# Optimization experiments

Hardware: AMD Instinct MI355X
Metric: run time of the kernel (lower is better)

Reference implementation:

```python
import jax, jax.numpy as jnp
import numpy as np

B, L, H, N = 32, 4096, 256, 512
THR = 0.0          # sim_threshold
NEG = -1e9         # mask value for softmax
SLOPE = 0.2        # LeakyReLU negative slope
EPS = 1e-8         # torch cosine_similarity eps


def _span_mean(cs, st, ed):
    # cs: [B, L+1, H] inclusive prefix sums with leading zero row
    hi = jnp.take_along_axis(cs, (ed + 1)[:, :, None], axis=1)  # [B,N,H]
    lo = jnp.take_along_axis(cs, st[:, :, None], axis=1)
    cnt = (ed - st + 1).astype(cs.dtype)[:, :, None]
    return (hi - lo) / cnt


def _leaky(x):
    return jnp.where(x >= 0, x, SLOPE * x)


def _forward(embeddings, W_trip, b_trip, edge_emb, W_attn, b_attn, W_gat, b_gat,
             asp_st, asp_len, opi_st, opi_len, sent_id):
    Bv, Lv, Hv = embeddings.shape
    asp_ed = asp_st + asp_len  # [B,N], always < L by construction
    opi_ed = opi_st + opi_len

    # span means via prefix sums (replaces per-triplet slice .mean(0))
    cs = jnp.concatenate([jnp.zeros((Bv, 1, Hv), embeddings.dtype),
                          jnp.cumsum(embeddings, axis=1)], axis=1)  # [B,L+1,H]
    asp_repr = _span_mean(cs, asp_st, asp_ed)  # [B,N,H]
    opi_repr = _span_mean(cs, opi_st, opi_ed)
    sent_vec = jax.nn.one_hot(sent_id, 3, dtype=embeddings.dtype)  # [B,N,3]

    node_in = jnp.concatenate([asp_repr, opi_repr, sent_vec], axis=-1)  # [B,N,2H+3]
    node = node_in @ W_trip + b_trip  # [B,N,H] triplet_proj

    # pairwise cosine similarity (torch eps semantics)
    nrm = jnp.sqrt(jnp.sum(node * node, axis=-1))  # [B,N]
    dots = jnp.einsum('bih,bjh->bij', node, node)
    sim = dots / jnp.maximum(nrm[:, :, None] * nrm[:, None, :], EPS)  # [B,N,N]

    eye = jnp.eye(N, dtype=bool)[None]
    same_asp = (asp_st[:, :, None] == asp_st[:, None, :]) & (asp_ed[:, :, None] == asp_ed[:, None, :])
    same_opi = (opi_st[:, :, None] == opi_st[:, None, :]) & (opi_ed[:, :, None] == opi_ed[:, None, :])
    pass_sim = (sim > THR) & ~eye
    mask0 = pass_sim & same_asp  # edge (src=i, tgt=j), type 0
    mask1 = pass_sim & same_opi  # type 1
    # em[b, tgt, src, type]
    em = jnp.stack([jnp.swapaxes(mask0, 1, 2), jnp.swapaxes(mask1, 1, 2)], axis=-1)

    # attn_fc(leaky_relu(concat[node_tgt, node_src, edge_emb])) decomposes linearly
    lnode = _leaky(node)            # [B,N,H]
    ledge = _leaky(edge_emb)        # [2,H]
    a_tgt = (lnode @ W_attn[:H]).squeeze(-1)        # [B,N]
    a_src = (lnode @ W_attn[H:2 * H]).squeeze(-1)   # [B,N]
    a_e = (ledge @ W_attn[2 * H:]).squeeze(-1)      # [2]
    score = (a_tgt[:, :, None, None] + a_src[:, None, :, None]
             + a_e[None, None, None, :] + b_attn[0])  # [B,N,N,2]

    masked = jnp.where(em, score, NEG)
    w = jax.nn.softmax(masked.reshape(Bv, N, -1), axis=-1).reshape(Bv, N, N, 2)
    w = w * em.astype(w.dtype)  # exact zeros on non-edges / neighborless rows

    # aggregate msgs = concat[node_src, edge_emb[type]]
    w_node = w.sum(-1)                                   # [B,tgt,src]
    agg_node = jnp.einsum('bki,bih->bkh', w_node, node)  # [B,N,H]
    agg_e = w.sum(2) @ edge_emb                          # [B,N,H]
    agg = jnp.concatenate([agg_node, agg_e], axis=-1)    # [B,N,2H]
    upd = jax.nn.relu(agg @ W_gat + b_gat)               # gat_proj + relu

    has_neigh = em.any(axis=(2, 3))                      # [B,N]
    node_out = jnp.where(has_neigh[:, :, None], upd, node)

    # original skips the whole batch element if it has no edges at all
    b_has_edge = em.any(axis=(1, 2, 3))                  # [B]
    node_add = jnp.where(b_has_edge[:, None, None], node_out, 0.0)

    center = (asp_st + opi_st) // 2                      # [B,N], < L
    b_idx = jnp.broadcast_to(jnp.arange(Bv)[:, None], center.shape)
    enhanced = embeddings.at[b_idx, center].add(node_add)
    return enhanced


def setup_inputs() -> dict:
    key = jax.random.key(0)
    ks = jax.random.split(key, 12)
    embeddings = jax.random.normal(ks[0], (B, L, H), jnp.float32)
    W_trip = jax.random.normal(ks[1], (2 * H + 3, H), jnp.float32) * 0.05
    b_trip = jnp.zeros((H,), jnp.float32)
    edge_emb = jax.random.normal(ks[2], (2, H), jnp.float32) * 0.05
    W_attn = jax.random.normal(ks[3], (3 * H, 1), jnp.float32) * 0.05
    b_attn = jnp.zeros((1,), jnp.float32)
    W_gat = jax.random.normal(ks[4], (2 * H, H), jnp.float32) * 0.05
    b_gat = jnp.zeros((H,), jnp.float32)
    asp_st = jax.random.randint(ks[5], (B, N), 0, 128, dtype=jnp.int32)
    asp_len = jax.random.randint(ks[6], (B, N), 0, 8, dtype=jnp.int32)
    opi_st = jax.random.randint(ks[7], (B, N), 0, 128, dtype=jnp.int32)
    opi_len = jax.random.randint(ks[8], (B, N), 0, 8, dtype=jnp.int32)
    sent_id = jax.random.randint(ks[9], (B, N), 0, 3, dtype=jnp.int32)
    return dict(embeddings=embeddings, W_trip=W_trip, b_trip=b_trip, edge_emb=edge_emb,
                W_attn=W_attn, b_attn=b_attn, W_gat=W_gat, b_gat=b_gat,
                asp_st=asp_st, asp_len=asp_len, opi_st=opi_st, opi_len=opi_len,
                sent_id=sent_id)


def reference(embeddings, W_trip, b_trip, edge_emb, W_attn, b_attn, W_gat, b_gat,
              asp_st, asp_len, opi_st, opi_len, sent_id):
    return _forward(embeddings, W_trip, b_trip, edge_emb, W_attn, b_attn, W_gat, b_gat,
                    asp_st, asp_len, opi_st, opi_len, sent_id)
```

## Files before the change

### kernel.cpp

```cpp
#include <hip/hip_runtime.h>
#include <hip/hip_bf16.h>
#include <math.h>

#define Bn 32
#define Ln 4096
#define ROWS 16384
#define LR 136
#define SLOPEC 0.2f
#define NEGSENT -1e30f

typedef __attribute__((ext_vector_type(8))) short bf16x8;
typedef __attribute__((ext_vector_type(4))) float f32x4;

__device__ __forceinline__ void copy_lin(const float* __restrict__ emb,
        float* __restrict__ out, long start, int count, int tid) {
    const f32x4* s4 = (const f32x4*)emb;
    f32x4* d4 = (f32x4*)out;
    for (int i = tid; i < count; i += 256)
        d4[start + i] = s4[start + i];
}

__device__ __forceinline__ f32x4 leaky4(f32x4 v) {
    f32x4 r;
    r.x = v.x >= 0.f ? v.x : SLOPEC * v.x;
    r.y = v.y >= 0.f ? v.y : SLOPEC * v.y;
    r.z = v.z >= 0.f ? v.z : SLOPEC * v.z;
    r.w = v.w >= 0.f ? v.w : SLOPEC * v.w;
    return r;
}

__global__ __launch_bounds__(256) void k_pre(const float* __restrict__ Wtrip,
        const float* __restrict__ btrip, const float* __restrict__ Eemb,
        const float* __restrict__ Wattn, const float* __restrict__ Wgat,
        const int* __restrict__ ast, const int* __restrict__ alen,
        const int* __restrict__ ost, const int* __restrict__ olen,
        const float* __restrict__ emb, float* __restrict__ out,
        __hip_bfloat16* __restrict__ WtGT, __hip_bfloat16* __restrict__ embh,
        float* __restrict__ W3g, float* __restrict__ btg,
        float* __restrict__ ae, float* __restrict__ ve,
        int* __restrict__ keys, int* __restrict__ bflag) {
    int bid = blockIdx.x, tid = threadIdx.x;
    copy_lin(emb, out, (long)bid * 864, 864, tid);
    __shared__ float Als[32][68];
    __shared__ float Bls[32][64];
    __shared__ float red[4];
    __shared__ float vr0[8][32], vr1[8][32];
    if (bid < 32) {
        int mat = bid >> 4, t = bid & 15;
        int m0 = (t >> 2) << 6, n0 = (t & 3) << 6;
        const float* A = Wtrip + mat * 65536;
        int r0 = (tid & 15) << 2, c0 = (tid >> 4) << 2;
        float acc[4][4] = {};
        for (int kk = 0; kk < 256; kk += 32) {
            __syncthreads();
            #pragma unroll
            for (int p = 0; p < 2; ++p) {
                int idx = tid + (p << 8);
                int row = idx >> 3, kq = (idx & 7) << 2;
                const float4 v = *(const float4*)(A + (size_t)(m0 + row) * 256 + kk + kq);
                Als[kq + 0][row] = v.x; Als[kq + 1][row] = v.y;
                Als[kq + 2][row] = v.z; Als[kq + 3][row] = v.w;
            }
            #pragma unroll
            for (int p = 0; p < 2; ++p) {
                int idx = tid + (p << 8);
                int k = idx >> 4, hq = (idx & 15) << 2;
                *(float4*)(&Bls[k][hq]) = *(const float4*)(Wgat + (size_t)(kk + k) * 256 + n0 + hq);
            }
            __syncthreads();
            #pragma unroll
            for (int k = 0; k < 32; ++k) {
                float4 a  = *(const float4*)(&Als[k][r0]);
                float4 bv = *(const float4*)(&Bls[k][c0]);
                acc[0][0] += a.x*bv.x; acc[0][1] += a.x*bv.y; acc[0][2] += a.x*bv.z; acc[0][3] += a.x*bv.w;
                acc[1][0] += a.y*bv.x; acc[1][1] += a.y*bv.y; acc[1][2] += a.y*bv.z; acc[1][3] += a.y*bv.w;
                acc[2][0] += a.z*bv.x; acc[2][1] += a.z*bv.y; acc[2][2] += a.z*bv.z; acc[2][3] += a.z*bv.w;
                acc[3][0] += a.w*bv.x; acc[3][1] += a.w*bv.y; acc[3][2] += a.w*bv.z; acc[3][3] += a.w*bv.w;
            }
        }
        #pragma unroll
        for (int i = 0; i < 4; ++i)
            #pragma unroll
            for (int j = 0; j < 4; ++j)
                WtGT[(size_t)(mat * 256 + n0 + c0 + j) * 256 + m0 + r0 + i] =
                    __float2bfloat16(acc[i][j]);
    } else if (bid == 32) {
        float s = 0.f;
        for (int k = 0; k < 256; ++k) s += btrip[k] * Wgat[(size_t)k * 256 + tid];
        btg[tid] = s;
    } else if (bid == 33) {
        if (tid < Bn) bflag[tid] = 0;
        #pragma unroll
        for (int e = 0; e < 2; ++e) {
            float x = Eemb[e * 256 + tid];
            float lx = x >= 0.f ? x : SLOPEC * x;
            float s = lx * Wattn[512 + tid];
            #pragma unroll
            for (int o = 32; o; o >>= 1) s += __shfl_down(s, o);
            if ((tid & 63) == 0) red[tid >> 6] = s;
            __syncthreads();
            if (tid == 0) ae[e] = red[0] + red[1] + red[2] + red[3];
            __syncthreads();
        }
    } else if (bid < 37) {
        int s = bid - 34;
        float acc = 0.f;
        for (int k = 0; k < 256; ++k)
            acc += Wtrip[(size_t)(512 + s) * 256 + k] * Wgat[(size_t)k * 256 + tid];
        W3g[s * 256 + tid] = acc;
    } else if (bid < 45) {
        int j = bid - 37;
        int n0 = j << 5;
        int nl = tid & 31, kg = tid >> 5;
        float p0 = 0.f, p1 = 0.f;
        for (int kk = 0; kk < 32; ++kk) {
            int k = (kg << 5) + kk;
            float w = Wgat[(size_t)(256 + k) * 256 + n0 + nl];
            p0 += Eemb[k] * w;
            p1 += Eemb[256 + k] * w;
        }
        vr0[kg][nl] = p0; vr1[kg][nl] = p1;
        __syncthreads();
        if (tid < 32) {
            float s0 = 0.f, s1 = 0.f;
            #pragma unroll
            for (int g = 0; g < 8; ++g) { s0 += vr0[g][tid]; s1 += vr1[g][tid]; }
            ve[n0 + tid] = s0;
            ve[256 + n0 + tid] = s1;
        }
    } else if (bid < 109) {
        int row = (bid - 45) * 256 + tid;
        keys[row] = (((ast[row] << 3) | alen[row]) << 10) | ((ost[row] << 3) | olen[row]);
    } else if (bid < 126) {
        int rbase = (bid - 109) << 8;
        int b2 = rbase / LR, l2 = rbase - b2 * LR;
        for (int r = 0; r < 256; ++r) {
            embh[(size_t)(rbase + r) * 256 + tid] =
                __float2bfloat16(emb[((size_t)b2 * Ln + l2) * 256 + tid]);
            if (++l2 == LR) { l2 = 0; ++b2; }
        }
    }
}

__global__ __launch_bounds__(256) void k_pq(const float* __restrict__ emb,
        const float* __restrict__ Wtrip,
        const __hip_bfloat16* __restrict__ embh, const __hip_bfloat16* __restrict__ WtGT,
        float* __restrict__ PQ, float* __restrict__ PQ2, float* __restrict__ out) {
    __shared__ float Als[32][68];
    __shared__ float Bls[32][64];
    int tid = threadIdx.x;
    int bid = blockIdx.x;
    copy_lin(emb, out, 884736L + (long)bid * 2048, 2048, tid);

    if (bid < 544) {
        int m0 = (bid % 68) << 6;
        int j = bid / 68;
        const float* Bp = Wtrip + ((j < 4) ? (j << 6) : (65536 + ((j - 4) << 6)));
        int r0 = (tid & 15) << 2;
        int c0 = (tid >> 4) << 2;
        float acc[4][4] = {};
        for (int kk = 0; kk < 256; kk += 32) {
            __syncthreads();
            #pragma unroll
            for (int p = 0; p < 2; ++p) {
                int idx = tid + (p << 8);
                int row = idx >> 3;
                int kq = (idx & 7) << 2;
                int m = m0 + row;
                int b = m / LR;
                int l = m - b * LR;
                const float4 v = *(const float4*)(emb + (size_t)(b * Ln + l) * 256 + kk + kq);
                Als[kq + 0][row] = v.x; Als[kq + 1][row] = v.y;
                Als[kq + 2][row] = v.z; Als[kq + 3][row] = v.w;
            }
            #pragma unroll
            for (int p = 0; p < 2; ++p) {
                int idx = tid + (p << 8);
                int k = idx >> 4;
                int hq = (idx & 15) << 2;
                *(float4*)(&Bls[k][hq]) = *(const float4*)(Bp + (size_t)(kk + k) * 256 + hq);
            }
            __syncthreads();
            #pragma unroll
            for (int k = 0; k < 32; ++k) {
                float4 a  = *(const float4*)(&Als[k][r0]);
                float4 bv = *(const float4*)(&Bls[k][c0]);
                acc[0][0] += a.x*bv.x; acc[0][1] += a.x*bv.y; acc[0][2] += a.x*bv.z; acc[0][3] += a.x*bv.w;
                acc[1][0] += a.y*bv.x; acc[1][1] += a.y*bv.y; acc[1][2] += a.y*bv.z; acc[1][3] += a.y*bv.w;
                acc[2][0] += a.z*bv.x; acc[2][1] += a.z*bv.y; acc[2][2] += a.z*bv.z; acc[2][3] += a.z*bv.w;
                acc[3][0] += a.w*bv.x; acc[3][1] += a.w*bv.y; acc[3][2] += a.w*bv.z; acc[3][3] += a.w*bv.w;
            }
        }
        #pragma unroll
        for (int i = 0; i < 4; ++i)
            #pragma unroll
            for (int jj = 0; jj < 4; ++jj)
                PQ[(size_t)(m0 + r0 + i) * 512 + (j << 6) + c0 + jj] = acc[i][jj];
    } else {
        int bb = bid - 544;
        int wave = tid >> 6, lane = tid & 63;
        int m0 = ((bb % 68) << 6) + (wave << 4);
        int n0 = (bb / 68) << 6;
        int fr = lane & 15;
        int kq = (lane >> 4) << 3;
        f32x4 acc[4] = {};
        for (int k0 = 0; k0 < 256; k0 += 32) {
            bf16x8 a = *(const bf16x8*)(embh + (size_t)(m0 + fr) * 256 + k0 + kq);
            #pragma unroll
            for (int nf = 0; nf < 4; ++nf) {
                bf16x8 b = *(const bf16x8*)(WtGT + (size_t)(n0 + (nf << 4) + fr) * 256 + k0 + kq);
                acc[nf] = __builtin_amdgcn_mfma_f32_16x16x32_bf16(a, b, acc[nf], 0, 0, 0);
            }
        }
        int r0 = (lane >> 4) << 2;
        #pragma unroll
        for (int nf = 0; nf < 4; ++nf)
            #pragma unroll
            for (int r = 0; r < 4; ++r)
                PQ2[(size_t)(m0 + r0 + r) * 512 + n0 + (nf << 4) + fr] = acc[nf][r];
    }
}

__global__ __launch_bounds__(256) void k_combine(const float* __restrict__ PQ,
        const float* __restrict__ PQ2,
        const float* __restrict__ Wtrip, const float* __restrict__ btrip,
        const int* __restrict__ sid,
        const int* __restrict__ ast, const int* __restrict__ alen,
        const int* __restrict__ ost, const int* __restrict__ olen,
        const float* __restrict__ Wattn, const float* __restrict__ W3g,
        const float* __restrict__ btg, const float* __restrict__ emb,
        float* __restrict__ out, float* __restrict__ node, float* __restrict__ nodeW,
        float* __restrict__ atg, float* __restrict__ asr) {
    int bid = blockIdx.x, tid = threadIdx.x;
    int wv = tid >> 6, lane = tid & 63;
    copy_lin(emb, out, 3112960L + (long)bid * 512, 512, tid);

    int row = (bid << 2) + wv;
    int b = row >> 9;
    int as_ = ast[row], al = alen[row];
    int os_ = ost[row], ol = olen[row];
    int c = lane << 2;
    const float* Pb  = PQ  + (size_t)b * LR * 512 + c;
    const float* Pb2 = PQ2 + (size_t)b * LR * 512 + c;

    f32x4 asum = {0.f,0.f,0.f,0.f}, osum = asum, p2 = asum, q2 = asum;
    for (int i = 0; i <= al; ++i) {
        size_t off = (size_t)(as_ + i) * 512;
        asum += *(const f32x4*)(Pb + off);
        p2   += *(const f32x4*)(Pb2 + off);
    }
    for (int i = 0; i <= ol; ++i) {
        size_t off = (size_t)(os_ + i) * 512 + 256;
        osum += *(const f32x4*)(Pb + off);
        q2   += *(const f32x4*)(Pb2 + off);
    }
    float ra = 1.f / (float)(al + 1), ro = 1.f / (float)(ol + 1);
    int sd = sid[row];

    f32x4 x = asum * ra + osum * ro
            + *(const f32x4*)(Wtrip + (size_t)(512 + sd) * 256 + c)
            + *(const f32x4*)(btrip + c);
    *(f32x4*)(node + (size_t)row * 256 + c) = x;

    f32x4 nw = p2 * ra + q2 * ro
             + *(const f32x4*)(W3g + sd * 256 + c)
             + *(const f32x4*)(btg + c);
    *(f32x4*)(nodeW + (size_t)row * 256 + c) = nw;

    f32x4 lx = leaky4(x);
    f32x4 w1 = *(const f32x4*)(Wattn + c);
    f32x4 w2 = *(const f32x4*)(Wattn + 256 + c);
    float s1 = lx.x*w1.x + lx.y*w1.y + lx.z*w1.z + lx.w*w1.w;
    float s2 = lx.x*w2.x + lx.y*w2.y + lx.z*w2.z + lx.w*w2.w;
    #pragma unroll
    for (int o = 32; o; o >>= 1) {
        s1 += __shfl_xor(s1, o);
        s2 += __shfl_xor(s2, o);
    }
    if (lane == 0) { atg[row] = s1; asr[row] = s2; }
}

__global__ __launch_bounds__(256) void k_edges(
        const float* __restrict__ node, const float* __restrict__ nodeW,
        const float* __restrict__ atg, const float* __restrict__ asr,
        const float* __restrict__ ae, const float* __restrict__ battn,
        const float* __restrict__ ve, const float* __restrict__ bgat,
        const int* __restrict__ keys,
        const float* __restrict__ emb, float* __restrict__ out,
        float* __restrict__ nadd, int* __restrict__ bflag) {
    int bid = blockIdx.x;
    int tid = threadIdx.x;
    int wv = tid >> 6, lane = tid & 63;

    copy_lin(emb, out, 5210112L + (long)bid * 776, 776, tid);

    int tgt = (bid << 2) + wv;
    int b = tgt >> 9, base = b << 9, lt = tgt & 511;

    int mykey = keys[tgt];
    int ka = mykey >> 10, ko = mykey & 1023;

    unsigned long long mA[8], mO[8];
    #pragma unroll
    for (int j = 0; j < 8; ++j) {
        int ls = (j << 6) + lane;
        int k2 = keys[base + ls];
        bool self = (ls == lt);
        mA[j] = __ballot(((k2 >> 10) == ka) && !self);
        mO[j] = __ballot(((k2 & 1023) == ko) && !self);
    }

    f32x4 xt4 = *(const f32x4*)(node + (size_t)tgt * 256 + (lane << 2));
    float a_t = atg[tgt];
    float ae0 = ae[0], ae1 = ae[1], b0 = battn[0];

    float s0a[8], s1a[8];
    unsigned long long mK[8];
    #pragma unroll
    for (int j = 0; j < 8; ++j) {
        s0a[j] = NEGSENT; s1a[j] = NEGSENT;
        unsigned long long m = mA[j] | mO[j];
        while (m) {
            int bit = __builtin_ctzll(m); m &= m - 1;
            int gs = base + (j << 6) + bit;
            f32x4 y = *(const f32x4*)(node + (size_t)gs * 256 + (lane << 2));
            float p = xt4.x * y.x + xt4.y * y.y + xt4.z * y.z + xt4.w * y.w;
            #pragma unroll
            for (int o = 32; o; o >>= 1) p += __shfl_xor(p, o);
            if (p > 0.f && lane == bit) {
                float bs = a_t + asr[gs] + b0;
                if ((mA[j] >> bit) & 1) s0a[j] = bs + ae0;
                if ((mO[j] >> bit) & 1) s1a[j] = bs + ae1;
            }
        }
        mK[j] = __ballot(s0a[j] > -1e29f || s1a[j] > -1e29f);
    }

    float mx = NEGSENT;
    #pragma unroll
    for (int j = 0; j < 8; ++j) mx = fmaxf(mx, fmaxf(s0a[j], s1a[j]));
    #pragma unroll
    for (int o = 32; o; o >>= 1) mx = fmaxf(mx, __shfl_xor(mx, o));
    bool has = mx > -1e29f;

    float se0 = 0.f, se1 = 0.f;
    #pragma unroll
    for (int j = 0; j < 8; ++j) {
        se0 += expf(s0a[j] - mx);
        se1 += expf(s1a[j] - mx);
    }
    #pragma unroll
    for (int o = 32; o; o >>= 1) { se0 += __shfl_xor(se0, o); se1 += __shfl_xor(se1, o); }
    float rden = 1.f / (se0 + se1);

    f32x4 res;
    if (has) {
        f32x4 agg4 = {0.f, 0.f, 0.f, 0.f};
        #pragma unroll
        for (int j = 0; j < 8; ++j) {
            unsigned long long m = mK[j];
            while (m) {
                int bit = __builtin_ctzll(m); m &= m - 1;
                int gs = base + (j << 6) + bit;
                float w0 = __shfl(s0a[j], bit);
                float w1 = __shfl(s1a[j], bit);
                float wt = (expf(w0 - mx) + expf(w1 - mx)) * rden;
                const f32x4 nw = *(const f32x4*)(nodeW + (size_t)gs * 256 + (lane << 2));
                agg4.x += wt * nw.x; agg4.y += wt * nw.y;
                agg4.z += wt * nw.z; agg4.w += wt * nw.w;
            }
        }
        f32x4 v1 = *(const f32x4*)(ve + (lane << 2));
        f32x4 v2 = *(const f32x4*)(ve + 256 + (lane << 2));
        f32x4 bg = *(const f32x4*)(bgat + (lane << 2));
        float c0 = se0 * rden, c1 = se1 * rden;
        res.x = fmaxf(agg4.x + c0 * v1.x + c1 * v2.x + bg.x, 0.f);
        res.y = fmaxf(agg4.y + c0 * v1.y + c1 * v2.y + bg.y, 0.f);
        res.z = fmaxf(agg4.z + c0 * v1.z + c1 * v2.z + bg.z, 0.f);
        res.w = fmaxf(agg4.w + c0 * v1.w + c1 * v2.w + bg.w, 0.f);
        if (lane == 0) bflag[b] = 1;
    } else {
        res = xt4;
    }
    *(f32x4*)(nadd + (size_t)tgt * 256 + (lane << 2)) = res;
}

__global__ __launch_bounds__(256) void k_scatter(const float* __restrict__ emb,
        const float* __restrict__ nadd,
        const int* __restrict__ ast, const int* __restrict__ ost,
        const int* __restrict__ bflag, float* __restrict__ out) {
    int b = blockIdx.x >> 7;
    int r = blockIdx.x & 127;
    int tid = threadIdx.x;

    __shared__ int cen[512];
    __shared__ unsigned long long s_mask[8];
    for (int n = tid; n < 512; n += 256)
        cen[n] = (ast[(b << 9) + n] + ost[(b << 9) + n]) >> 1;
    __syncthreads();
    #pragma unroll
    for (int p = 0; p < 2; ++p) {
        int n = tid + (p << 8);
        unsigned long long bal = __ballot(cen[n] == r);
        if ((tid & 63) == 0) s_mask[(p << 2) + (tid >> 6)] = bal;
    }
    __syncthreads();
    size_t o = ((size_t)b * Ln + r) * 256 + tid;
    float acc = emb[o];
    if (bflag[b]) {
        for (int w = 0; w < 8; ++w) {
            unsigned long long m = s_mask[w];
            while (m) {
                int n = (w << 6) + __builtin_ctzll(m); m &= m - 1;
                acc += nadd[((size_t)(b << 9) + n) * 256 + tid];
            }
        }
    }
    out[o] = acc;
}

extern "C" void kernel_launch(void* const* d_in, const int* in_sizes, int n_in,
                              void* d_out, int out_size, void* d_ws, size_t ws_size,
                              hipStream_t stream) {
    const float* emb   = (const float*)d_in[0];
    const float* Wtrip = (const float*)d_in[1];
    const float* btrip = (const float*)d_in[2];
    const float* Eemb  = (const float*)d_in[3];
    const float* Wattn = (const float*)d_in[4];
    const float* battn = (const float*)d_in[5];
    const float* Wgat  = (const float*)d_in[6];
    const float* bgat  = (const float*)d_in[7];
    const int* ast  = (const int*)d_in[8];
    const int* alen = (const int*)d_in[9];
    const int* ost  = (const int*)d_in[10];
    const int* olen = (const int*)d_in[11];
    const int* sid  = (const int*)d_in[12];
    float* out = (float*)d_out;

    float* ws    = (float*)d_ws;
    float* PQ    = ws;
    float* PQ2   = PQ + (size_t)4352 * 512;
    float* node  = PQ2 + (size_t)4352 * 512;
    float* nodeW = node + (size_t)ROWS * 256;
    float* nadd  = nodeW + (size_t)ROWS * 256;
    float* W3g   = nadd + (size_t)ROWS * 256;
    float* btg   = W3g + 768;
    float* atg   = btg + 256;
    float* asr   = atg + ROWS;
    float* ae    = asr + ROWS;
    float* ve    = ae + 2;
    int* bflag   = (int*)(ve + 512);
    int* keys    = bflag + Bn;
    __hip_bfloat16* embh = (__hip_bfloat16*)(keys + ROWS + 32);
    __hip_bfloat16* WtGT = embh + (size_t)4352 * 256;

    k_pre<<<1024, 256, 0, stream>>>(Wtrip, btrip, Eemb, Wattn, Wgat,
                                    ast, alen, ost, olen, emb, out,
                                    WtGT, embh, W3g, btg, ae, ve, keys, bflag);
    k_pq<<<1088, 256, 0, stream>>>(emb, Wtrip, embh, WtGT, PQ, PQ2, out);
    k_combine<<<ROWS / 4, 256, 0, stream>>>(PQ, PQ2, Wtrip, btrip, sid,
                                            ast, alen, ost, olen,
                                            Wattn, W3g, btg, emb, out, node, nodeW,
                                            atg, asr);
    k_edges<<<ROWS / 4, 256, 0, stream>>>(node, nodeW, atg, asr, ae, battn, ve, bgat,
                                          keys, emb, out, nadd, bflag);
    k_scatter<<<Bn * 128, 256, 0, stream>>>(emb, nadd, ast, ost, bflag, out);
}
```

Baseline: 157.9 us.

## Fuse scatter into edge kernel via atomics and repartition output copy

Removes the separate scatter kernel and the nadd buffer: each target row's updated node vector is atomically added into the output at its span-center row. The copy of embeddings into the output is redistributed so the first 128 rows per batch are copied before k_edges runs. A small fix-up kernel subtracts node contributions for batches with no edges. k_combine and k_edges blocks are also remapped to interleave batches. This trades a full extra kernel pass and nadd traffic for float atomics, which are contended on shared center rows and make the summation order nondeterministic.

New measurement: 179.0 us. 1.13x slower.

```diff
diff --git a/kernel.cpp b/kernel.cpp
--- a/kernel.cpp
+++ b/kernel.cpp
@@ -40,7 +40,20 @@
         float* __restrict__ ae, float* __restrict__ ve,
         int* __restrict__ keys, int* __restrict__ bflag) {
     int bid = blockIdx.x, tid = threadIdx.x;
-    copy_lin(emb, out, (long)bid * 864, 864, tid);
+    copy_lin(emb, out, (long)bid * 1536, 1536, tid);
+    {
+        const f32x4* s4 = (const f32x4*)emb;
+        f32x4* d4 = (f32x4*)out;
+        #pragma unroll
+        for (int i = 0; i < 64; i += 256) {}
+        int s2base = bid * 64;
+        #pragma unroll
+        for (int i = tid; i < 64; i += 256) {
+            long s2 = s2base + i;
+            long slot = ((24L + (s2 >> 13)) << 18) | (s2 & 8191);
+            d4[slot] = s4[slot];
+        }
+    }
     __shared__ float Als[32][68];
     __shared__ float Bls[32][64];
     __shared__ float red[4];
@@ -150,7 +163,7 @@
     __shared__ float Bls[32][64];
     int tid = threadIdx.x;
     int bid = blockIdx.x;
-    copy_lin(emb, out, 884736L + (long)bid * 2048, 2048, tid);
+    copy_lin(emb, out, 1572864L + (long)bid * 2048, 2048, tid);
 
     if (bid < 544) {
         int m0 = (bid % 68) << 6;
@@ -233,9 +246,10 @@
         float* __restrict__ atg, float* __restrict__ asr) {
     int bid = blockIdx.x, tid = threadIdx.x;
     int wv = tid >> 6, lane = tid & 63;
-    copy_lin(emb, out, 3112960L + (long)bid * 512, 512, tid);
-
-    int row = (bid << 2) + wv;
+    copy_lin(emb, out, 3801088L + (long)bid * 608, 608, tid);
+
+    int s = ((bid & 7) << 9) | (bid >> 3);
+    int row = (s << 2) + wv;
     int b = row >> 9;
     int as_ = ast[row], al = alen[row];
     int os_ = ost[row], ol = olen[row];
@@ -286,15 +300,23 @@
         const float* __restrict__ ae, const float* __restrict__ battn,
         const float* __restrict__ ve, const float* __restrict__ bgat,
         const int* __restrict__ keys,
+        const int* __restrict__ ast, const int* __restrict__ ost,
         const float* __restrict__ emb, float* __restrict__ out,
-        float* __restrict__ nadd, int* __restrict__ bflag) {
+        int* __restrict__ bflag) {
     int bid = blockIdx.x;
     int tid = threadIdx.x;
     int wv = tid >> 6, lane = tid & 63;
 
-    copy_lin(emb, out, 5210112L + (long)bid * 776, 776, tid);
-
-    int tgt = (bid << 2) + wv;
+    {
+        const f32x4* s4 = (const f32x4*)emb;
+        f32x4* d4 = (f32x4*)out;
+        long base = ((24L + (bid >> 9)) << 18) + 8192 + (long)(bid & 511) * 496;
+        for (int i = tid; i < 496; i += 256)
+            d4[base + i] = s4[base + i];
+    }
+
+    int s = ((bid & 7) << 9) | (bid >> 3);
+    int tgt = (s << 2) + wv;
     int b = tgt >> 9, base = b << 9, lt = tgt & 511;
 
     int mykey = keys[tgt];
@@ -382,41 +404,26 @@
     } else {
         res = xt4;
     }
-    *(f32x4*)(nadd + (size_t)tgt * 256 + (lane << 2)) = res;
-}
-
-__global__ __launch_bounds__(256) void k_scatter(const float* __restrict__ emb,
-        const float* __restrict__ nadd,
+    int cen = (ast[tgt] + ost[tgt]) >> 1;
+    float* orow = out + ((size_t)b * Ln + cen) * 256 + (lane << 2);
+    atomicAdd(orow + 0, res.x);
+    atomicAdd(orow + 1, res.y);
+    atomicAdd(orow + 2, res.z);
+    atomicAdd(orow + 3, res.w);
+}
+
+__global__ __launch_bounds__(256) void k_fix(const float* __restrict__ node,
         const int* __restrict__ ast, const int* __restrict__ ost,
         const int* __restrict__ bflag, float* __restrict__ out) {
-    int b = blockIdx.x >> 7;
-    int r = blockIdx.x & 127;
+    int b = blockIdx.x;
+    if (bflag[b]) return;
     int tid = threadIdx.x;
-
-    __shared__ int cen[512];
-    __shared__ unsigned long long s_mask[8];
-    for (int n = tid; n < 512; n += 256)
-        cen[n] = (ast[(b << 9) + n] + ost[(b << 9) + n]) >> 1;
-    __syncthreads();
-    #pragma unroll
-    for (int p = 0; p < 2; ++p) {
-        int n = tid + (p << 8);
-        unsigned long long bal = __ballot(cen[n] == r);
-        if ((tid & 63) == 0) s_mask[(p << 2) + (tid >> 6)] = bal;
-    }
-    __syncthreads();
-    size_t o = ((size_t)b * Ln + r) * 256 + tid;
-    float acc = emb[o];
-    if (bflag[b]) {
-        for (int w = 0; w < 8; ++w) {
-            unsigned long long m = s_mask[w];
-            while (m) {
-                int n = (w << 6) + __builtin_ctzll(m); m &= m - 1;
-                acc += nadd[((size_t)(b << 9) + n) * 256 + tid];
-            }
-        }
-    }
-    out[o] = acc;
+    for (int n = 0; n < 512; ++n) {
+        int row = (b << 9) + n;
+        int cen = (ast[row] + ost[row]) >> 1;
+        atomicAdd(&out[((size_t)b * Ln + cen) * 256 + tid],
+                  -node[(size_t)row * 256 + tid]);
+    }
 }
 
 extern "C" void kernel_launch(void* const* d_in, const int* in_sizes, int n_in,
@@ -442,8 +449,7 @@
     float* PQ2   = PQ + (size_t)4352 * 512;
     float* node  = PQ2 + (size_t)4352 * 512;
     float* nodeW = node + (size_t)ROWS * 256;
-    float* nadd  = nodeW + (size_t)ROWS * 256;
-    float* W3g   = nadd + (size_t)ROWS * 256;
+    float* W3g   = nodeW + (size_t)ROWS * 256;
     float* btg   = W3g + 768;
     float* atg   = btg + 256;
     float* asr   = atg + ROWS;
@@ -463,6 +469,6 @@
                                             Wattn, W3g, btg, emb, out, node, nodeW,
                                             atg, asr);
     k_edges<<<ROWS / 4, 256, 0, stream>>>(node, nodeW, atg, asr, ae, battn, ve, bgat,
-                                          keys, emb, out, nadd, bflag);
-    k_scatter<<<Bn * 128, 256, 0, stream>>>(emb, nadd, ast, ost, bflag, out);
-}
+                                          keys, ast, ost, emb, out, bflag);
+    k_fix<<<Bn, 256, 0, stream>>>(node, ast, ost, bflag, out);
+}
```
